# Optimization experiments

Measured on AMD Instinct MI355X. Metric: run time of the kernel, lower is better.

## Reference

```python
import jax, jax.numpy as jnp
import numpy as np

B, D, F = 2048, 512, 16384
K = 3
AUX_THR = 0.7
EPS = 1e-8


def setup_inputs() -> dict:
    key = jax.random.key(0)
    ks = jax.random.split(key, 14)
    sc_e = 1.0 / np.sqrt(D)
    sc_d = 1.0 / np.sqrt(F)
    return {
        "model_activations": jax.random.normal(ks[0], (B, D), jnp.float32),
        "We": jax.random.normal(ks[1], (F, D), jnp.float32) * sc_e,
        "be": jax.random.normal(ks[2], (F,), jnp.float32) * 0.01,
        "Wd": jax.random.normal(ks[3], (D, F), jnp.float32) * sc_d,
        "bd": jax.random.normal(ks[4], (D,), jnp.float32) * 0.01,
        "We1": jax.random.normal(ks[5], (F, D), jnp.float32) * sc_e,
        "be1": jax.random.normal(ks[6], (F,), jnp.float32) * 0.01,
        "Wd1": jax.random.normal(ks[7], (D, F), jnp.float32) * sc_d,
        "bd1": jax.random.normal(ks[8], (D,), jnp.float32) * 0.01,
        "We2": jax.random.normal(ks[9], (F, D), jnp.float32) * sc_e,
        "be2": jax.random.normal(ks[10], (F,), jnp.float32) * 0.01,
        "Wd2": jax.random.normal(ks[11], (D, F), jnp.float32) * sc_d,
        "bd2": jax.random.normal(ks[12], (D,), jnp.float32) * 0.01,
    }


def _forward(x, We, be, Wd, bd, We1, be1, Wd1, bd1, We2, be2, Wd2, bd2):
    # parent encoder + top-k scatter
    pre = x @ We.T + be                                   # [B, F]
    vals, idx = jax.lax.top_k(pre, K)                     # [B, K]
    sae = jnp.zeros_like(pre).at[jnp.arange(B)[:, None], idx].set(vals)

    # child routing
    pre1 = x @ We1.T + be1
    pre2 = x @ We2.T + be2
    sae_nz = sae != 0.0
    m1 = jnp.where(sae_nz, pre1, 0.0)
    m2 = jnp.where(sae_nz, pre2, 0.0)
    winners = m1 > m2
    fa1 = jnp.where(winners, m1, 0.0)
    fa2 = jnp.where(~winners, m2, 0.0)

    recon = (sae @ Wd.T + bd) + (fa1 @ Wd1.T + bd1) + (fa2 @ Wd2.T + bd2)

    # live-latent counts (as arrays, jit-friendly)
    n_parent = jnp.zeros((F,), jnp.float32).at[idx.reshape(-1)].set(1.0).sum().astype(jnp.int32)
    n_c1 = jnp.any(fa1 != 0, axis=0).sum().astype(jnp.int32)
    n_c2 = jnp.any(fa2 != 0, axis=0).sum().astype(jnp.int32)

    # auxiliary cosine loss, computed per-feature without materializing
    # the [B, D, F] scaled_parent / combined_weights tensors:
    #   scaled_parent[b,:,f] = a * Wd[:,f],  scaled_child[b,:,f] = c * Wc[:,f]
    # cos over D reduces to per-feature Gram terms.
    pp = jnp.sum(Wd * Wd, axis=0)      # [F] ||Wp_f||^2
    p1 = jnp.sum(Wd * Wd1, axis=0)     # [F] Wp_f . W1_f
    p2 = jnp.sum(Wd * Wd2, axis=0)
    s11 = jnp.sum(Wd1 * Wd1, axis=0)
    s22 = jnp.sum(Wd2 * Wd2, axis=0)

    a = sae                                              # [B, F]
    c = jnp.where(winners, fa1, fa2)                     # [B, F]
    pc = jnp.where(winners, p1[None, :], p2[None, :])    # [B, F]
    cc = jnp.where(winners, s11[None, :], s22[None, :])

    dot = a * (a * pp[None, :] + c * pc)                 # <scaled_parent, combined>
    nx = jnp.abs(a) * jnp.sqrt(pp)[None, :]              # ||scaled_parent||
    ny2 = a * a * pp[None, :] + 2.0 * a * c * pc + c * c * cc
    ny = jnp.sqrt(jnp.maximum(ny2, 0.0))                 # ||combined||
    cos = dot / (jnp.maximum(nx, EPS) * jnp.maximum(ny, EPS))

    active = (a > 0).astype(cos.dtype)
    sim_loss = jnp.maximum(0.0, AUX_THR - cos) * active
    aux = sim_loss.sum() / (active.sum() + 1e-08)

    return recon, (n_parent, n_c1, n_c2), aux


def reference(model_activations, We, be, Wd, bd, We1, be1, Wd1, bd1, We2, be2, Wd2, bd2):
    return _forward(model_activations, We, be, Wd, bd, We1, be1, Wd1, bd1, We2, be2, Wd2, bd2)
```

## Files before the change

kernel.cpp:

```cpp
#include <hip/hip_runtime.h>
#include <math.h>

#define B_DIM 2048
#define D_DIM 512
#define F_DIM 16384
#define K_TOP 3

typedef __attribute__((ext_vector_type(8))) short bf16x8;
typedef __attribute__((ext_vector_type(4))) float f32x4;

#define GL16(gsrc, ldst) \
  __builtin_amdgcn_global_load_lds( \
      (__attribute__((address_space(1))) const void*)(gsrc), \
      (__attribute__((address_space(3))) void*)(ldst), 16, 0, 0)

#define WAITVMCNT(n) asm volatile("s_waitcnt vmcnt(" #n ")" ::: "memory")
#define BARRIER() do { asm volatile("" ::: "memory"); \
    __builtin_amdgcn_s_barrier(); \
    asm volatile("" ::: "memory"); } while (0)

__device__ __forceinline__ bool better(float v, int c, float w, int j) {
    return (v > w) || (v == w && c < j);
}

__device__ __forceinline__ void ins3(float v, int c,
    float& v0, int& i0, float& v1, int& i1, float& v2, int& i2)
{
    if (!better(v, c, v2, i2)) return;
    if (better(v, c, v1, i1)) {
        v2 = v1; i2 = i1;
        if (better(v, c, v0, i0)) { v1 = v0; i1 = i0; v0 = v; i0 = c; }
        else { v1 = v; i1 = c; }
    } else { v2 = v; i2 = c; }
}

__device__ __forceinline__ uint okey(uint b16, int col) {
    uint m = 0x8000u + ((b16 >> 15) * 0x7FFFu);
    return ((b16 ^ m) << 14) | (uint)(16383 - col);
}

__device__ __forceinline__ void insK8(uint k, uint* V) {
#pragma unroll
    for (int j = 0; j < 8; ++j) {
        uint hi = V[j] > k ? V[j] : k;
        uint lo = V[j] > k ? k : V[j];
        V[j] = hi; k = lo;
    }
}

__device__ __forceinline__ void insK3(uint k, uint& V0, uint& V1, uint& V2) {
    uint h0 = V0 > k ? V0 : k, l0 = V0 > k ? k : V0; V0 = h0; k = l0;
    uint h1 = V1 > k ? V1 : k, l1 = V1 > k ? k : V1; V1 = h1; k = l1;
    V2 = V2 > k ? V2 : k;
}

__device__ __forceinline__ float bf2f(ushort u) {
    return __uint_as_float((uint)u << 16);
}

__global__ __launch_bounds__(256) void convert_kernel(
    const float* __restrict__ We, ushort* __restrict__ We_bf,
    const float* __restrict__ x, ushort* __restrict__ x_bf)
{
    const float* src; ushort* dst; int n8, i, stride;
    if (blockIdx.x < 2048) {
        src = We; dst = We_bf; n8 = F_DIM * D_DIM / 8;
        i = blockIdx.x * 256 + threadIdx.x; stride = 2048 * 256;
    } else {
        src = x; dst = x_bf; n8 = B_DIM * D_DIM / 8;
        i = (blockIdx.x - 2048) * 256 + threadIdx.x; stride = 256 * 256;
    }
    for (; i < n8; i += stride) {
        float4 a = ((const float4*)src)[i * 2];
        float4 b = ((const float4*)src)[i * 2 + 1];
        uint4 o;
        o.x = (__float_as_uint(a.y) & 0xFFFF0000u) | (__float_as_uint(a.x) >> 16);
        o.y = (__float_as_uint(a.w) & 0xFFFF0000u) | (__float_as_uint(a.z) >> 16);
        o.z = (__float_as_uint(b.y) & 0xFFFF0000u) | (__float_as_uint(b.x) >> 16);
        o.w = (__float_as_uint(b.w) & 0xFFFF0000u) | (__float_as_uint(b.z) >> 16);
        ((uint4*)dst)[i] = o;
    }
}

__global__ __launch_bounds__(256) void gemm_kernel(
    const ushort* __restrict__ xb, const ushort* __restrict__ web,
    const float* __restrict__ be, uint* __restrict__ packed)
{
    __shared__ __align__(16) ushort As[2][4096];
    __shared__ __align__(16) ushort Bs[2][4096];

    const int t = threadIdx.x;
    const int id = blockIdx.x;
    const int r = id & 127;
    const int bx = ((r & 7) << 4) + (r >> 3);
    const int by = id >> 7;
    const int l = t & 63;
    const int w = t >> 6;
    const int wr = w >> 1, wc = w & 1;
    const int bm0 = by << 7;
    const int fn0 = bx << 7;
    const int frow = l & 15;
    const int q = l >> 4;

    const int srow = t >> 2;
    const int sgr = (t & 3) ^ ((t >> 3) & 3);
    const int soff = sgr << 3;
    const ushort* gA0 = xb + (size_t)(bm0 + srow) * D_DIM + soff;
    const ushort* gA1 = xb + (size_t)(bm0 + 64 + srow) * D_DIM + soff;
    const ushort* gB0 = web + (size_t)(fn0 + srow) * D_DIM + soff;
    const ushort* gB1 = web + (size_t)(fn0 + 64 + srow) * D_DIM + soff;

#define STAGE(bufp, koff) do { \
    GL16(gA0 + (koff), (char*)As + (bufp) * 8192 + t * 16); \
    GL16(gA1 + (koff), (char*)As + (bufp) * 8192 + 4096 + t * 16); \
    GL16(gB0 + (koff), (char*)Bs + (bufp) * 8192 + t * 16); \
    GL16(gB1 + (koff), (char*)Bs + (bufp) * 8192 + 4096 + t * 16); \
} while (0)

    f32x4 acc[4][4];
#pragma unroll
    for (int m = 0; m < 4; ++m)
#pragma unroll
        for (int n = 0; n < 4; ++n) acc[m][n] = (f32x4)(0.f);

    const int qs = (q ^ ((frow >> 1) & 3)) << 3;
    const int aoff = (wr * 64 + frow) * 32 + qs;
    const int boff = (wc * 64 + frow) * 32 + qs;

    STAGE(0, 0);

#pragma unroll 1
    for (int t16 = 0; t16 < 16; ++t16) {
        const int cur = t16 & 1;
        if (t16 < 15) {
            STAGE(cur ^ 1, (t16 + 1) * 32);
            WAITVMCNT(4);
        } else {
            WAITVMCNT(0);
        }
        BARRIER();
        const ushort* Ab = &As[0][0] + cur * 4096 + aoff;
        const ushort* Bb = &Bs[0][0] + cur * 4096 + boff;
        bf16x8 af[4], bfr[4];
#pragma unroll
        for (int m = 0; m < 4; ++m) af[m] = *(const bf16x8*)(Ab + m * 512);
#pragma unroll
        for (int n = 0; n < 4; ++n) bfr[n] = *(const bf16x8*)(Bb + n * 512);
#pragma unroll
        for (int m = 0; m < 4; ++m)
#pragma unroll
            for (int n = 0; n < 4; ++n)
                acc[m][n] = __builtin_amdgcn_mfma_f32_16x16x32_bf16(
                    af[m], bfr[n], acc[m][n], 0, 0, 0);
        BARRIER();
    }
#undef STAGE

    float bias[4];
#pragma unroll
    for (int n = 0; n < 4; ++n) bias[n] = be[fn0 + wc * 64 + n * 16 + frow];

    const int colb = fn0 + wc * 64 + frow;
    const int rowbase = bm0 + wr * 64 + (q << 2);
    const int tile2 = (bx << 1) + wc;
#pragma unroll
    for (int m = 0; m < 4; ++m) {
#pragma unroll
        for (int i = 0; i < 4; ++i) {
            uint V0 = 0, V1 = 0, V2 = 0;
#pragma unroll
            for (int n = 0; n < 4; ++n) {
                float v = acc[m][n][i] + bias[n];
                uint key = okey(__float_as_uint(v) >> 16, colb + n * 16);
                insK3(key, V0, V1, V2);
            }
#pragma unroll
            for (int mk = 1; mk <= 8; mk <<= 1) {
                uint o0 = (uint)__shfl_xor((int)V0, mk);
                uint o1 = (uint)__shfl_xor((int)V1, mk);
                uint o2 = (uint)__shfl_xor((int)V2, mk);
                insK3(o0, V0, V1, V2);
                insK3(o1, V0, V1, V2);
                insK3(o2, V0, V1, V2);
            }
            if (frow == 0) {
                uint* dp = packed + (size_t)(rowbase + m * 16 + i) * 768 + tile2 * 3;
                dp[0] = V0; dp[1] = V1; dp[2] = V2;
            }
        }
    }
}

__global__ __launch_bounds__(512) void trgram_kernel(
    const float* __restrict__ Wd, const float* __restrict__ Wd1,
    const float* __restrict__ Wd2, ushort* __restrict__ WdT,
    ushort* __restrict__ Wd1T, ushort* __restrict__ Wd2T,
    float* __restrict__ gram, int* __restrict__ flags3F)
{
    if (threadIdx.x < 48)
        ((uint4*)flags3F)[blockIdx.x * 48 + threadIdx.x] = make_uint4(0, 0, 0, 0);

    __shared__ float tA[64][65], tB[64][65], tC[64][65];
    __shared__ float gred[8][64][5];
    const int t = threadIdx.x;
    const int f0 = blockIdx.x << 6;
    const int wg = t >> 6;
    const int fl = t & 63;
    float pp = 0, p1 = 0, p2 = 0, s11 = 0, s22 = 0;

    for (int ch = 0; ch < 8; ++ch) {
        const int d0 = ch << 6;
        float a[8], b[8], c[8];
#pragma unroll
        for (int it = 0; it < 8; ++it) {
            int dl = (it << 3) + wg;
            size_t off = (size_t)(d0 + dl) * F_DIM + f0 + fl;
            a[it] = Wd[off]; b[it] = Wd1[off]; c[it] = Wd2[off];
        }
        if (ch) __syncthreads();
#pragma unroll
        for (int it = 0; it < 8; ++it) {
            pp  = fmaf(a[it], a[it], pp);
            p1  = fmaf(a[it], b[it], p1);
            p2  = fmaf(a[it], c[it], p2);
            s11 = fmaf(b[it], b[it], s11);
            s22 = fmaf(c[it], c[it], s22);
            int dl = (it << 3) + wg;
            tA[dl][fl] = a[it]; tB[dl][fl] = b[it]; tC[dl][fl] = c[it];
        }
        __syncthreads();
#pragma unroll
        for (int it = 0; it < 8; ++it) {
            int flw = (it << 3) + wg, dlw = fl;
            size_t doff = (size_t)(f0 + flw) * D_DIM + d0 + dlw;
            WdT[doff]  = (ushort)(__float_as_uint(tA[dlw][flw]) >> 16);
            Wd1T[doff] = (ushort)(__float_as_uint(tB[dlw][flw]) >> 16);
            Wd2T[doff] = (ushort)(__float_as_uint(tC[dlw][flw]) >> 16);
        }
    }
    gred[wg][fl][0] = pp;  gred[wg][fl][1] = p1; gred[wg][fl][2] = p2;
    gred[wg][fl][3] = s11; gred[wg][fl][4] = s22;
    __syncthreads();
    if (t < 64) {
        float g0 = 0, g1 = 0, g2 = 0, g3 = 0, g4 = 0;
#pragma unroll
        for (int g = 0; g < 8; ++g) {
            g0 += gred[g][t][0]; g1 += gred[g][t][1]; g2 += gred[g][t][2];
            g3 += gred[g][t][3]; g4 += gred[g][t][4];
        }
        gram[f0 + t] = g0;
        gram[F_DIM + f0 + t] = g1;
        gram[2 * F_DIM + f0 + t] = g2;
        gram[3 * F_DIM + f0 + t] = g3;
        gram[4 * F_DIM + f0 + t] = g4;
    }
}

__global__ __launch_bounds__(512) void mrcra_kernel(
    const uint* __restrict__ packed,
    const float* __restrict__ x, const float* __restrict__ We,
    const float* __restrict__ be,
    const float* __restrict__ We1, const float* __restrict__ be1,
    const float* __restrict__ We2, const float* __restrict__ be2,
    const float* __restrict__ gram,
    const ushort* __restrict__ WdT, const float* __restrict__ bd,
    const ushort* __restrict__ Wd1T, const float* __restrict__ bd1,
    const ushort* __restrict__ Wd2T, const float* __restrict__ bd2,
    int* __restrict__ flagP, int* __restrict__ flag1, int* __restrict__ flag2,
    float* __restrict__ auxpart, float* __restrict__ cntpart,
    float* __restrict__ out)
{
    __shared__ int sc8[8];
    __shared__ float sv[8];
    __shared__ int si[8];
    __shared__ float sval[3], sdot[3][2], scv[3], sterm[3], sact[3];
    __shared__ int sidx[3], swin[3];
    const int row = blockIdx.x;
    const int t = threadIdx.x;
    const int wv = t >> 6, l = t & 63;

    if (t < 64) {
        const uint* p = packed + (size_t)row * 768;
        uint V[8] = {0, 0, 0, 0, 0, 0, 0, 0};
#pragma unroll
        for (int m = 0; m < 12; ++m) {
            uint k = p[t + (m << 6)];
            if (k > V[7]) insK8(k, V);
        }
#pragma unroll
        for (int mk = 1; mk < 64; mk <<= 1) {
            uint o[8];
#pragma unroll
            for (int j = 0; j < 8; ++j) o[j] = (uint)__shfl_xor((int)V[j], mk);
#pragma unroll
            for (int j = 0; j < 8; ++j)
                if (o[j] > V[7]) insK8(o[j], V);
        }
        if (t == 0) {
#pragma unroll
            for (int j = 0; j < 8; ++j)
                sc8[j] = 16383 - (int)(V[j] & 16383u);
        }
    }
    __syncthreads();

    {
        const int f = sc8[wv];
        const float* xr = x + (size_t)row * D_DIM;
        const float* wp = We + (size_t)f * D_DIM;
        float s = 0.f;
#pragma unroll
        for (int m = 0; m < 8; ++m) { int e = l + (m << 6); s = fmaf(xr[e], wp[e], s); }
#pragma unroll
        for (int mk = 1; mk < 64; mk <<= 1) s += __shfl_xor(s, mk);
        if (l == 0) { sv[wv] = s + be[f]; si[wv] = f; }
    }
    __syncthreads();
    if (t == 0) {
        float v0 = -INFINITY, v1 = -INFINITY, v2 = -INFINITY;
        int i0 = 0x7fffffff, i1 = 0x7fffffff, i2 = 0x7fffffff;
        for (int k = 0; k < 8; ++k) ins3(sv[k], si[k], v0, i0, v1, i1, v2, i2);
        sval[0] = v0; sidx[0] = i0;
        sval[1] = v1; sidx[1] = i1;
        sval[2] = v2; sidx[2] = i2;
    }
    __syncthreads();

    if (wv < 6) {
        const int p = wv >> 1, mt = wv & 1;
        const int f = sidx[p];
        const float* wp = (mt ? We2 : We1) + (size_t)f * D_DIM;
        const float* xr = x + (size_t)row * D_DIM;
        float s = 0.f;
#pragma unroll
        for (int m = 0; m < 8; ++m) { int e = l + (m << 6); s = fmaf(xr[e], wp[e], s); }
#pragma unroll
        for (int mk = 1; mk < 64; mk <<= 1) s += __shfl_xor(s, mk);
        if (l == 0) sdot[p][mt] = s + (mt ? be2 : be1)[f];
    }
    __syncthreads();

    if (t < 3) {
        const int p = t;
        const float a = sval[p];
        const int f = sidx[p];
        float m1 = (a != 0.f) ? sdot[p][0] : 0.f;
        float m2 = (a != 0.f) ? sdot[p][1] : 0.f;
        bool win = m1 > m2;
        float fa1 = win ? m1 : 0.f;
        float fa2 = win ? 0.f : m2;
        float cv = win ? fa1 : fa2;
        scv[p] = cv; swin[p] = win ? 1 : 0;
        flagP[f] = 1;
        if (fa1 != 0.f) flag1[f] = 1;
        if (fa2 != 0.f) flag2[f] = 1;
        const float pp = gram[f];
        const float pc = win ? gram[F_DIM + f] : gram[2 * F_DIM + f];
        const float cc = win ? gram[3 * F_DIM + f] : gram[4 * F_DIM + f];
        const float dot = a * (a * pp + cv * pc);
        const float nx = fabsf(a) * sqrtf(pp);
        const float ny2 = a * a * pp + 2.f * a * cv * pc + cv * cv * cc;
        const float ny = sqrtf(fmaxf(ny2, 0.f));
        const float cosv = dot / (fmaxf(nx, 1e-8f) * fmaxf(ny, 1e-8f));
        sterm[p] = (a > 0.f) ? fmaxf(0.f, 0.7f - cosv) : 0.f;
        sact[p] = (a > 0.f) ? 1.f : 0.f;
    }
    __syncthreads();
    if (t == 0) {
        auxpart[row] = sterm[0] + sterm[1] + sterm[2];
        cntpart[row] = sact[0] + sact[1] + sact[2];
    }

    const int d = t;
    float o = bd[d] + bd1[d] + bd2[d];
#pragma unroll
    for (int k = 0; k < 3; ++k) {
        const int f = sidx[k];
        const float a = sval[k];
        const float c = scv[k];
        const int win = swin[k];
        const size_t off = (size_t)f * D_DIM + d;
        o = fmaf(a, bf2f(WdT[off]), o);
        if (c != 0.f) {
            const ushort* wt = win ? Wd1T : Wd2T;
            o = fmaf(c, bf2f(wt[off]), o);
        }
    }
    out[(size_t)row * D_DIM + d] = o;
}

__global__ __launch_bounds__(256) void finalize_kernel(
    const int* __restrict__ flagP, const int* __restrict__ flag1,
    const int* __restrict__ flag2,
    const float* __restrict__ auxpart, const float* __restrict__ cntpart,
    float* __restrict__ out)
{
    const int t = threadIdx.x;
    int sp = 0, s1 = 0, s2 = 0;
    for (int f = t; f < F_DIM; f += 256) { sp += flagP[f]; s1 += flag1[f]; s2 += flag2[f]; }
    float asum = 0.f, acnt = 0.f;
    for (int i = t; i < B_DIM; i += 256) { asum += auxpart[i]; acnt += cntpart[i]; }
#pragma unroll
    for (int m = 1; m < 64; m <<= 1) {
        sp += __shfl_xor(sp, m); s1 += __shfl_xor(s1, m); s2 += __shfl_xor(s2, m);
        asum += __shfl_xor(asum, m); acnt += __shfl_xor(acnt, m);
    }
    __shared__ int red[3][4];
    __shared__ float fred[2][4];
    const int w = t >> 6;
    if ((t & 63) == 0) {
        red[0][w] = sp; red[1][w] = s1; red[2][w] = s2;
        fred[0][w] = asum; fred[1][w] = acnt;
    }
    __syncthreads();
    if (t == 0) {
        float np_ = (float)(red[0][0] + red[0][1] + red[0][2] + red[0][3]);
        float n1_ = (float)(red[1][0] + red[1][1] + red[1][2] + red[1][3]);
        float n2_ = (float)(red[2][0] + red[2][1] + red[2][2] + red[2][3]);
        float as = fred[0][0] + fred[0][1] + fred[0][2] + fred[0][3];
        float ac = fred[1][0] + fred[1][1] + fred[1][2] + fred[1][3];
        const size_t base = (size_t)B_DIM * D_DIM;
        out[base + 0] = np_;
        out[base + 1] = n1_;
        out[base + 2] = n2_;
        out[base + 3] = as / (ac + 1e-8f);
    }
}

extern "C" void kernel_launch(void* const* d_in, const int* in_sizes, int n_in,
                              void* d_out, int out_size, void* d_ws, size_t ws_size,
                              hipStream_t stream)
{
    (void)in_sizes; (void)n_in; (void)out_size; (void)ws_size;
    const float* x   = (const float*)d_in[0];
    const float* We  = (const float*)d_in[1];
    const float* be  = (const float*)d_in[2];
    const float* Wd  = (const float*)d_in[3];
    const float* bd  = (const float*)d_in[4];
    const float* We1 = (const float*)d_in[5];
    const float* be1 = (const float*)d_in[6];
    const float* Wd1 = (const float*)d_in[7];
    const float* bd1 = (const float*)d_in[8];
    const float* We2 = (const float*)d_in[9];
    const float* be2 = (const float*)d_in[10];
    const float* Wd2 = (const float*)d_in[11];
    const float* bd2 = (const float*)d_in[12];
    float* out = (float*)d_out;

    ushort* x_bf  = (ushort*)d_ws;
    ushort* We_bf = x_bf + (size_t)B_DIM * D_DIM;
    ushort* WdT   = We_bf + (size_t)F_DIM * D_DIM;
    ushort* Wd1T  = WdT + (size_t)F_DIM * D_DIM;
    ushort* Wd2T  = Wd1T + (size_t)F_DIM * D_DIM;
    uint*   packed = (uint*)(Wd2T + (size_t)F_DIM * D_DIM);
    float*  gram  = (float*)(packed + (size_t)B_DIM * 768);
    int*    flagP = (int*)(gram + 5 * F_DIM);
    int*    flag1 = flagP + F_DIM;
    int*    flag2 = flag1 + F_DIM;
    float*  auxpart = (float*)(flag2 + F_DIM);
    float*  cntpart = auxpart + B_DIM;

    convert_kernel<<<2304, 256, 0, stream>>>(We, We_bf, x, x_bf);

    gemm_kernel<<<2048, 256, 0, stream>>>(x_bf, We_bf, be, packed);

    trgram_kernel<<<F_DIM / 64, 512, 0, stream>>>(
        Wd, Wd1, Wd2, WdT, Wd1T, Wd2T, gram, flagP);

    mrcra_kernel<<<B_DIM, 512, 0, stream>>>(
        packed, x, We, be, We1, be1, We2, be2, gram,
        WdT, bd, Wd1T, bd1, Wd2T, bd2,
        flagP, flag1, flag2, auxpart, cntpart, out);

    finalize_kernel<<<1, 256, 0, stream>>>(
        flagP, flag1, flag2, auxpart, cntpart, out);
}
```

Before: 136.6 us.

## Fuse fp32-to-bf16 conversion of encoder weights into GEMM tile staging

Drops the separate pass that converted We to bf16 and instead loads fp32 We tiles in the GEMM, packs them to bf16 in registers and stores them swizzled into LDS. This removes a full read and write of the encoder weights before the GEMM. In exchange, the GEMM reads twice as many bytes per B tile across all row blocks, and B staging now goes through registers instead of the asynchronous global-to-LDS path.

```diff
diff --git a/kernel.cpp b/kernel.cpp
--- a/kernel.cpp
+++ b/kernel.cpp
@@ -13,11 +13,6 @@
   __builtin_amdgcn_global_load_lds( \
       (__attribute__((address_space(1))) const void*)(gsrc), \
       (__attribute__((address_space(3))) void*)(ldst), 16, 0, 0)
-
-#define WAITVMCNT(n) asm volatile("s_waitcnt vmcnt(" #n ")" ::: "memory")
-#define BARRIER() do { asm volatile("" ::: "memory"); \
-    __builtin_amdgcn_s_barrier(); \
-    asm volatile("" ::: "memory"); } while (0)
 
 __device__ __forceinline__ bool better(float v, int c, float w, int j) {
     return (v > w) || (v == w && c < j);
@@ -58,32 +53,30 @@
     return __uint_as_float((uint)u << 16);
 }
 
+__device__ __forceinline__ uint pk(uint lo, uint hi) {
+    return (hi & 0xFFFF0000u) | (lo >> 16);
+}
+
 __global__ __launch_bounds__(256) void convert_kernel(
-    const float* __restrict__ We, ushort* __restrict__ We_bf,
     const float* __restrict__ x, ushort* __restrict__ x_bf)
 {
-    const float* src; ushort* dst; int n8, i, stride;
-    if (blockIdx.x < 2048) {
-        src = We; dst = We_bf; n8 = F_DIM * D_DIM / 8;
-        i = blockIdx.x * 256 + threadIdx.x; stride = 2048 * 256;
-    } else {
-        src = x; dst = x_bf; n8 = B_DIM * D_DIM / 8;
-        i = (blockIdx.x - 2048) * 256 + threadIdx.x; stride = 256 * 256;
-    }
+    const int n8 = B_DIM * D_DIM / 8;
+    int i = blockIdx.x * 256 + threadIdx.x;
+    const int stride = 256 * 256;
     for (; i < n8; i += stride) {
-        float4 a = ((const float4*)src)[i * 2];
-        float4 b = ((const float4*)src)[i * 2 + 1];
+        float4 a = ((const float4*)x)[i * 2];
+        float4 b = ((const float4*)x)[i * 2 + 1];
         uint4 o;
-        o.x = (__float_as_uint(a.y) & 0xFFFF0000u) | (__float_as_uint(a.x) >> 16);
-        o.y = (__float_as_uint(a.w) & 0xFFFF0000u) | (__float_as_uint(a.z) >> 16);
-        o.z = (__float_as_uint(b.y) & 0xFFFF0000u) | (__float_as_uint(b.x) >> 16);
-        o.w = (__float_as_uint(b.w) & 0xFFFF0000u) | (__float_as_uint(b.z) >> 16);
-        ((uint4*)dst)[i] = o;
+        o.x = pk(__float_as_uint(a.x), __float_as_uint(a.y));
+        o.y = pk(__float_as_uint(a.z), __float_as_uint(a.w));
+        o.z = pk(__float_as_uint(b.x), __float_as_uint(b.y));
+        o.w = pk(__float_as_uint(b.z), __float_as_uint(b.w));
+        ((uint4*)x_bf)[i] = o;
     }
 }
 
 __global__ __launch_bounds__(256) void gemm_kernel(
-    const ushort* __restrict__ xb, const ushort* __restrict__ web,
+    const ushort* __restrict__ xb, const float* __restrict__ wef,
     const float* __restrict__ be, uint* __restrict__ packed)
 {
     __shared__ __align__(16) ushort As[2][4096];
@@ -103,42 +96,59 @@
     const int q = l >> 4;
 
     const int srow = t >> 2;
-    const int sgr = (t & 3) ^ ((t >> 3) & 3);
-    const int soff = sgr << 3;
-    const ushort* gA0 = xb + (size_t)(bm0 + srow) * D_DIM + soff;
-    const ushort* gA1 = xb + (size_t)(bm0 + 64 + srow) * D_DIM + soff;
-    const ushort* gB0 = web + (size_t)(fn0 + srow) * D_DIM + soff;
-    const ushort* gB1 = web + (size_t)(fn0 + 64 + srow) * D_DIM + soff;
-
-#define STAGE(bufp, koff) do { \
+    const int sg = t & 3;
+    const int key = (t >> 3) & 3;
+    const ushort* gA0 = xb + (size_t)(bm0 + srow) * D_DIM + ((sg ^ key) << 3);
+    const ushort* gA1 = xb + (size_t)(bm0 + 64 + srow) * D_DIM + ((sg ^ key) << 3);
+    const float* gB0 = wef + (size_t)(fn0 + srow) * D_DIM + (sg << 3);
+    const float* gB1 = wef + (size_t)(fn0 + 64 + srow) * D_DIM + (sg << 3);
+    char* wB0 = (char*)&Bs[0][0] + srow * 64 + ((sg ^ key) << 4);
+    char* wB1 = wB0 + 4096;
+
+#define STAGE_A(bufp, koff) do { \
     GL16(gA0 + (koff), (char*)As + (bufp) * 8192 + t * 16); \
     GL16(gA1 + (koff), (char*)As + (bufp) * 8192 + 4096 + t * 16); \
-    GL16(gB0 + (koff), (char*)Bs + (bufp) * 8192 + t * 16); \
-    GL16(gB1 + (koff), (char*)Bs + (bufp) * 8192 + 4096 + t * 16); \
 } while (0)
+#define LOADB(koff) do { \
+    bA = *(const uint4*)(gB0 + (koff)); \
+    bB = *(const uint4*)(gB0 + (koff) + 4); \
+    bC = *(const uint4*)(gB1 + (koff)); \
+    bD = *(const uint4*)(gB1 + (koff) + 4); \
+} while (0)
+#define CVTWRITE_B(bufp) do { \
+    uint4 w0, w1; \
+    w0.x = pk(bA.x, bA.y); w0.y = pk(bA.z, bA.w); \
+    w0.z = pk(bB.x, bB.y); w0.w = pk(bB.z, bB.w); \
+    w1.x = pk(bC.x, bC.y); w1.y = pk(bC.z, bC.w); \
+    w1.z = pk(bD.x, bD.y); w1.w = pk(bD.z, bD.w); \
+    *(uint4*)(wB0 + (bufp) * 8192) = w0; \
+    *(uint4*)(wB1 + (bufp) * 8192) = w1; \
+} while (0)
 
     f32x4 acc[4][4];
 #pragma unroll
     for (int m = 0; m < 4; ++m)
 #pragma unroll
         for (int n = 0; n < 4; ++n) acc[m][n] = (f32x4)(0.f);
+
+    uint4 bA, bB, bC, bD;
 
     const int qs = (q ^ ((frow >> 1) & 3)) << 3;
     const int aoff = (wr * 64 + frow) * 32 + qs;
     const int boff = (wc * 64 + frow) * 32 + qs;
 
-    STAGE(0, 0);
+    STAGE_A(0, 0);
+    LOADB(0);
+    CVTWRITE_B(0);
+    __syncthreads();
 
 #pragma unroll 1
     for (int t16 = 0; t16 < 16; ++t16) {
         const int cur = t16 & 1;
         if (t16 < 15) {
-            STAGE(cur ^ 1, (t16 + 1) * 32);
-            WAITVMCNT(4);
-        } else {
-            WAITVMCNT(0);
-        }
-        BARRIER();
+            STAGE_A(cur ^ 1, (t16 + 1) * 32);
+            LOADB((t16 + 1) * 32);
+        }
         const ushort* Ab = &As[0][0] + cur * 4096 + aoff;
         const ushort* Bb = &Bs[0][0] + cur * 4096 + boff;
         bf16x8 af[4], bfr[4];
@@ -152,9 +162,12 @@
             for (int n = 0; n < 4; ++n)
                 acc[m][n] = __builtin_amdgcn_mfma_f32_16x16x32_bf16(
                     af[m], bfr[n], acc[m][n], 0, 0, 0);
-        BARRIER();
-    }
-#undef STAGE
+        if (t16 < 15) CVTWRITE_B(cur ^ 1);
+        __syncthreads();
+    }
+#undef STAGE_A
+#undef LOADB
+#undef CVTWRITE_B
 
     float bias[4];
 #pragma unroll
@@ -171,8 +184,8 @@
 #pragma unroll
             for (int n = 0; n < 4; ++n) {
                 float v = acc[m][n][i] + bias[n];
-                uint key = okey(__float_as_uint(v) >> 16, colb + n * 16);
-                insK3(key, V0, V1, V2);
+                uint k2 = okey(__float_as_uint(v) >> 16, colb + n * 16);
+                insK3(k2, V0, V1, V2);
             }
 #pragma unroll
             for (int mk = 1; mk <= 8; mk <<= 1) {
@@ -460,9 +473,9 @@
     float*  auxpart = (float*)(flag2 + F_DIM);
     float*  cntpart = auxpart + B_DIM;
 
-    convert_kernel<<<2304, 256, 0, stream>>>(We, We_bf, x, x_bf);
-
-    gemm_kernel<<<2048, 256, 0, stream>>>(x_bf, We_bf, be, packed);
+    convert_kernel<<<256, 256, 0, stream>>>(x, x_bf);
+
+    gemm_kernel<<<2048, 256, 0, stream>>>(x_bf, We, be, packed);
 
     trgram_kernel<<<F_DIM / 64, 512, 0, stream>>>(
         Wd, Wd1, Wd2, WdT, Wd1T, Wd2T, gram, flagP);
```

New measurement: 150.4 us. 10.1% more time.
